# Kernel tuning notes

Hardware: AMD Instinct MI355X
Metric: run time of the kernel (lower is better)

The kernel has to match this reference:

```python
import jax, jax.numpy as jnp
import numpy as np

# ---- statevector quantum-circuit simulation helpers ----

def _rx(theta):
    # RX gate; theta scalar -> [2,2], theta [T] -> [T,2,2]
    c = jnp.cos(theta / 2.0).astype(jnp.complex64)
    s = (-1j * jnp.sin(theta / 2.0)).astype(jnp.complex64)
    return jnp.stack([jnp.stack([c, s], -1), jnp.stack([s, c], -1)], -2)


def _rot(phi, theta, omega):
    # PennyLane Rot = RZ(omega) RY(theta) RZ(phi)
    c = jnp.cos(theta / 2.0).astype(jnp.complex64)
    s = jnp.sin(theta / 2.0).astype(jnp.complex64)
    ep = jnp.exp(-0.5j * (omega + phi)).astype(jnp.complex64)
    em = jnp.exp(0.5j * (omega - phi)).astype(jnp.complex64)
    return jnp.stack([jnp.stack([ep * c, -jnp.conj(em) * s], -1),
                      jnp.stack([em * s, jnp.conj(ep) * c], -1)], -2)


def _apply1(state, gate, wire):
    # state: [T] + [2]*n ; gate: [2,2] (shared) or [T,2,2] (per-token encoding)
    state = jnp.moveaxis(state, 1 + wire, -1)
    if gate.ndim == 3:
        state = jnp.einsum('t...a,tba->t...b', state, gate)
    else:
        state = jnp.einsum('...a,ba->...b', state, gate)
    return jnp.moveaxis(state, -1, 1 + wire)


def _cnot(state, c, t):
    st = jnp.moveaxis(state, (1 + c, 1 + t), (-2, -1))
    st = jnp.stack([st[..., 0, :], st[..., 1, ::-1]], axis=-2)
    return jnp.moveaxis(st, (-2, -1), (1 + c, 1 + t))


def _zexp(state, wire):
    p = state.real ** 2 + state.imag ** 2
    p = jnp.moveaxis(p, 1 + wire, -1).reshape(p.shape[0], -1, 2)
    return jnp.sum(p[..., 0] - p[..., 1], axis=1)


def _qcircuit(x, w, scalar_out):
    # x: [T, n] angle-encoded inputs; w: [3n] (+1 if scalar_out) trainable angles
    T, n = x.shape
    state = jnp.zeros((T,) + (2,) * n, jnp.complex64)
    state = state.at[(slice(None),) + (0,) * n].set(1.0)
    for i in range(n):                       # angle encoding
        state = _apply1(state, _rx(x[:, i]), i)
    if n > 1:                                # ring entanglement
        for i in range(n):
            state = _cnot(state, i, (i + 1) % n)
    for i in range(n):                       # trainable rotations
        state = _apply1(state, _rot(w[3 * i], w[3 * i + 1], w[3 * i + 2]), i)
    if scalar_out:                           # query/key: extra RX, measure Z on wire 0
        state = _apply1(state, _rx(w[3 * n]), 0)
        return _zexp(state, 0)
    return jnp.stack([_zexp(state, i) for i in range(n)], axis=-1)


def _layernorm(x, eps=1e-5):
    m = jnp.mean(x, -1, keepdims=True)
    v = jnp.mean((x - m) ** 2, -1, keepdims=True)
    return (x - m) / jnp.sqrt(v + eps)


def setup_inputs() -> dict:
    key = jax.random.key(0)
    k = jax.random.split(key, 5)
    B, S, E, H = 16, 512, 8, 2
    d = E // H
    return {
        'x': jax.random.normal(k[0], (B, S, E), jnp.float32),
        'Vw': jax.random.normal(k[1], (H, 3 * d), jnp.float32),
        'Qw': jax.random.normal(k[2], (H, 3 * d + 1), jnp.float32),
        'Kw': jax.random.normal(k[3], (H, 3 * d + 1), jnp.float32),
        'Mw': jax.random.normal(k[4], (3 * E,), jnp.float32),
    }


def reference(x, Vw, Qw, Kw, Mw):
    B, S, E = x.shape
    H = Vw.shape[0]
    d = E // H
    scale = 1.0 / np.sqrt(d).astype(np.float32)
    xn = _layernorm(x)
    outs = []
    for h in range(H):  # fixed small loop over structurally distinct heads
        xh = xn[..., h * d:(h + 1) * d].reshape(B * S, d)
        V = _qcircuit(xh, Vw[h], False).reshape(B, S, d)
        Q = _qcircuit(xh, Qw[h], True).reshape(B, S)
        K = _qcircuit(xh, Kw[h], True).reshape(B, S)
        A = -(Q[:, :, None] - K[:, None, :]) ** 2          # [B,S,S]
        P = jax.nn.softmax(A * scale, axis=-1)
        outs.append(jnp.einsum('bij,bjd->bid', P, V))
    head_out = jnp.concatenate(outs, axis=-1)              # [B,S,E]
    merged = _qcircuit(head_out.reshape(B * S, E), Mw, False).reshape(B, S, E)
    return merged + x
```

## Files before the change

### kernel.cpp

```cpp
#include <hip/hip_runtime.h>

#define NS 512


__global__ __launch_bounds__(256)
void k_attn(const float* __restrict__ x, const float* __restrict__ Vw,
            const float* __restrict__ Qw, const float* __restrict__ Kw,
            float* __restrict__ HO)
{
    __shared__ float Qs[NS];
    __shared__ float Ks[NS];
    __shared__ float4 Vs[NS];

    int blk = blockIdx.x;
    int rg = blk & 31;
    int b  = (blk >> 5) & 15;
    int h  = blk >> 9;
    int tid = threadIdx.x;

    const float* qw = Qw + h*13;
    const float* kw = Kw + h*13;
    const float* vw = Vw + h*12;
    float sT, cT, sB, cB;
    __sincosf(qw[1], &sT, &cT); __sincosf(qw[12], &sB, &cB);
    float aQ = cB*cT + sB*sT*__sinf(qw[2]);
    __sincosf(kw[1], &sT, &cT); __sincosf(kw[12], &sB, &cB);
    float aK = cB*cT + sB*sT*__sinf(kw[2]);
    float vc0 = __cosf(vw[1]);
    float vc1 = __cosf(vw[4]);
    float vc2 = __cosf(vw[7]);
    float s3, vc3; __sincosf(vw[10], &s3, &vc3);
    float vs3 = s3 * __sinf(vw[9]);

    #pragma unroll
    for (int k = 0; k < 2; ++k) {
        int tl = tid + k*256;
        const float4* xp = (const float4*)(x + (b*NS + tl)*8);
        float4 xa = xp[0], xb = xp[1];
        float xv[8] = {xa.x, xa.y, xa.z, xa.w, xb.x, xb.y, xb.z, xb.w};
        float m = 0.f;
        #pragma unroll
        for (int e = 0; e < 8; ++e) m += xv[e];
        m *= 0.125f;
        float var = 0.f;
        #pragma unroll
        for (int e = 0; e < 8; ++e) { float d = xv[e]-m; var += d*d; }
        float inv = rsqrtf(var*0.125f + 1e-5f);

        float cg[4], sg[4];
        #pragma unroll
        for (int i = 0; i < 4; ++i)
            __sincosf((xv[h*4+i]-m)*inv, &sg[i], &cg[i]);

        float c01  = cg[0]*cg[1];
        float c123 = cg[1]*cg[2]*cg[3];
        Qs[tl] = aQ * c123;
        Ks[tl] = aK * c123;
        float4 v;
        v.x = vc0 * c123;
        v.y = vc1 * c01;
        v.z = vc2 * c01 * cg[2];
        v.w = vc3 * c01 * cg[2] * cg[3] + vs3 * sg[0]*sg[1]*sg[3]*cg[2];
        Vs[tl] = v;
    }
    __syncthreads();

    int lane = tid & 63;
    int w = tid >> 6;
    int g = lane >> 4;
    int l16 = lane & 15;
    int i = rg*16 + w*4 + g;
    float q = Qs[i];

    float sum = 0.f, a0 = 0.f, a1 = 0.f, a2 = 0.f, a3 = 0.f;
    #pragma unroll
    for (int k = 0; k < 32; ++k) {
        int j = k*16 + l16;
        float d = q - Ks[j];
        float p = __expf(-0.5f*d*d);
        float4 vv = Vs[j];
        sum += p; a0 += p*vv.x; a1 += p*vv.y; a2 += p*vv.z; a3 += p*vv.w;
    }
    #pragma unroll
    for (int off = 1; off < 16; off <<= 1) {
        sum += __shfl_xor(sum, off, 16);
        a0  += __shfl_xor(a0,  off, 16);
        a1  += __shfl_xor(a1,  off, 16);
        a2  += __shfl_xor(a2,  off, 16);
        a3  += __shfl_xor(a3,  off, 16);
    }
    if (l16 == 0) {
        float r = 1.0f / sum;
        float4 o = {a0*r, a1*r, a2*r, a3*r};
        *((float4*)(HO + ((b*NS + i))*8 + h*4)) = o;
    }
}

__global__ __launch_bounds__(64)
void k_merge(const float* __restrict__ HO, const float* __restrict__ x,
             const float* __restrict__ Mw, float* __restrict__ out)
{
    int t = blockIdx.x * 64 + threadIdx.x;

    float cT0 = __cosf(Mw[1]);
    float cT1 = __cosf(Mw[4]);
    float cT2 = __cosf(Mw[7]);
    float cT3 = __cosf(Mw[10]);
    float cT4 = __cosf(Mw[13]);
    float cT5 = __cosf(Mw[16]);
    float cT6 = __cosf(Mw[19]);
    float s7w, cT7; __sincosf(Mw[22], &s7w, &cT7);
    float vs77 = s7w * __sinf(Mw[21]);

    const float4* hp = (const float4*)(HO + t*8);
    float4 h0 = hp[0], h1 = hp[1];
    float a[8] = {h0.x, h0.y, h0.z, h0.w, h1.x, h1.y, h1.z, h1.w};

    float ca[8], sa0, sa1, sa7;
    __sincosf(a[0], &sa0, &ca[0]);
    __sincosf(a[1], &sa1, &ca[1]);
    ca[2] = __cosf(a[2]);
    ca[3] = __cosf(a[3]);
    ca[4] = __cosf(a[4]);
    ca[5] = __cosf(a[5]);
    ca[6] = __cosf(a[6]);
    __sincosf(a[7], &sa7, &ca[7]);

    float P1 = ca[0]*ca[1];
    float P2 = P1*ca[2];
    float P3 = P2*ca[3];
    float P4 = P3*ca[4];
    float P5 = P4*ca[5];
    float P6 = P5*ca[6];
    float P7 = P6*ca[7];
    float c34 = ca[3]*ca[4], c56 = ca[5]*ca[6];
    float Q17 = ca[1]*ca[2]*c34*c56*ca[7];
    float M26 = ca[2]*c34*c56;

    float e0 = cT0*Q17;
    float e1 = cT1*P1;
    float e2 = cT2*P2;
    float e3 = cT3*P3;
    float e4 = cT4*P4;
    float e5 = cT5*P5;
    float e6 = cT6*P6;
    float e7 = cT7*P7 + vs77 * sa0*sa1*sa7*M26;

    const float4* xp = (const float4*)(x + t*8);
    float4 x0 = xp[0], x1 = xp[1];
    float4 o0 = {e0 + x0.x, e1 + x0.y, e2 + x0.z, e3 + x0.w};
    float4 o1 = {e4 + x1.x, e5 + x1.y, e6 + x1.z, e7 + x1.w};
    float4* op = (float4*)(out + t*8);
    op[0] = o0; op[1] = o1;
}

extern "C" void kernel_launch(void* const* d_in, const int* in_sizes, int n_in,
                              void* d_out, int out_size, void* d_ws, size_t ws_size,
                              hipStream_t stream) {
    (void)in_sizes; (void)n_in; (void)out_size; (void)ws_size;
    const float* x  = (const float*)d_in[0];
    const float* Vw = (const float*)d_in[1];
    const float* Qw = (const float*)d_in[2];
    const float* Kw = (const float*)d_in[3];
    const float* Mw = (const float*)d_in[4];
    float* out = (float*)d_out;
    float* HO  = (float*)d_ws;

    hipLaunchKernelGGL(k_attn,  dim3(1024), dim3(256), 0, stream, x, Vw, Qw, Kw, HO);
    hipLaunchKernelGGL(k_merge, dim3(128),  dim3(64),  0, stream, HO, x, Mw, out);
}
```

Measured before the change: 12.70 us.

## Fuse attention heads and merge circuit into a single kernel

Combines the two attention heads and the merge quantum circuit into one kernel. Each block now handles one 16-row group of a batch for both heads, computing Q/K/V for both heads in shared memory and writing head outputs to shared memory instead of a global workspace. The merge circuit and residual add then run in the same block, removing the second launch and the global round trip. In exchange, per-block LDS usage doubles, each row is reduced by 8 lanes instead of 16 with a longer loop, and the merge stage runs on only 16 threads.

```diff
diff --git a/kernel.cpp b/kernel.cpp
--- a/kernel.cpp
+++ b/kernel.cpp
@@ -4,33 +4,36 @@
 
 
 __global__ __launch_bounds__(256)
-void k_attn(const float* __restrict__ x, const float* __restrict__ Vw,
-            const float* __restrict__ Qw, const float* __restrict__ Kw,
-            float* __restrict__ HO)
+void k_fused(const float* __restrict__ x, const float* __restrict__ Vw,
+             const float* __restrict__ Qw, const float* __restrict__ Kw,
+             const float* __restrict__ Mw, float* __restrict__ out)
 {
-    __shared__ float Qs[NS];
-    __shared__ float Ks[NS];
-    __shared__ float4 Vs[NS];
+    __shared__ float  Qs[2][NS];
+    __shared__ float  Ks[2][NS];
+    __shared__ float4 Vs[2][NS];
+    __shared__ float  HOs[16][8];
 
-    int blk = blockIdx.x;
-    int rg = blk & 31;
-    int b  = (blk >> 5) & 15;
-    int h  = blk >> 9;
     int tid = threadIdx.x;
+    int b   = blockIdx.x >> 5;
+    int rg  = blockIdx.x & 31;
 
-    const float* qw = Qw + h*13;
-    const float* kw = Kw + h*13;
-    const float* vw = Vw + h*12;
-    float sT, cT, sB, cB;
-    __sincosf(qw[1], &sT, &cT); __sincosf(qw[12], &sB, &cB);
-    float aQ = cB*cT + sB*sT*__sinf(qw[2]);
-    __sincosf(kw[1], &sT, &cT); __sincosf(kw[12], &sB, &cB);
-    float aK = cB*cT + sB*sT*__sinf(kw[2]);
-    float vc0 = __cosf(vw[1]);
-    float vc1 = __cosf(vw[4]);
-    float vc2 = __cosf(vw[7]);
-    float s3, vc3; __sincosf(vw[10], &s3, &vc3);
-    float vs3 = s3 * __sinf(vw[9]);
+    float aQ[2], aK[2], vc0[2], vc1[2], vc2[2], vc3[2], vs3[2];
+    #pragma unroll
+    for (int h = 0; h < 2; ++h) {
+        const float* qw = Qw + h*13;
+        const float* kw = Kw + h*13;
+        const float* vw = Vw + h*12;
+        float sT, cT, sB, cB;
+        __sincosf(qw[1], &sT, &cT); __sincosf(qw[12], &sB, &cB);
+        aQ[h] = cB*cT + sB*sT*__sinf(qw[2]);
+        __sincosf(kw[1], &sT, &cT); __sincosf(kw[12], &sB, &cB);
+        aK[h] = cB*cT + sB*sT*__sinf(kw[2]);
+        vc0[h] = __cosf(vw[1]);
+        vc1[h] = __cosf(vw[4]);
+        vc2[h] = __cosf(vw[7]);
+        float s3; __sincosf(vw[10], &s3, &vc3[h]);
+        vs3[h] = s3 * __sinf(vw[9]);
+    }
 
     #pragma unroll
     for (int k = 0; k < 2; ++k) {
@@ -47,125 +50,121 @@
         for (int e = 0; e < 8; ++e) { float d = xv[e]-m; var += d*d; }
         float inv = rsqrtf(var*0.125f + 1e-5f);
 
-        float cg[4], sg[4];
         #pragma unroll
-        for (int i = 0; i < 4; ++i)
-            __sincosf((xv[h*4+i]-m)*inv, &sg[i], &cg[i]);
-
-        float c01  = cg[0]*cg[1];
-        float c123 = cg[1]*cg[2]*cg[3];
-        Qs[tl] = aQ * c123;
-        Ks[tl] = aK * c123;
-        float4 v;
-        v.x = vc0 * c123;
-        v.y = vc1 * c01;
-        v.z = vc2 * c01 * cg[2];
-        v.w = vc3 * c01 * cg[2] * cg[3] + vs3 * sg[0]*sg[1]*sg[3]*cg[2];
-        Vs[tl] = v;
+        for (int h = 0; h < 2; ++h) {
+            float cg[4], sg[4];
+            #pragma unroll
+            for (int i = 0; i < 4; ++i)
+                __sincosf((xv[h*4+i]-m)*inv, &sg[i], &cg[i]);
+            float c01  = cg[0]*cg[1];
+            float c123 = cg[1]*cg[2]*cg[3];
+            Qs[h][tl] = aQ[h] * c123;
+            Ks[h][tl] = aK[h] * c123;
+            float4 v;
+            v.x = vc0[h] * c123;
+            v.y = vc1[h] * c01;
+            v.z = vc2[h] * c01 * cg[2];
+            v.w = vc3[h] * c01 * cg[2] * cg[3] + vs3[h] * sg[0]*sg[1]*sg[3]*cg[2];
+            Vs[h][tl] = v;
+        }
     }
     __syncthreads();
 
-    int lane = tid & 63;
-    int w = tid >> 6;
-    int g = lane >> 4;
-    int l16 = lane & 15;
-    int i = rg*16 + w*4 + g;
-    float q = Qs[i];
+    {
+        int lane = tid & 63;
+        int w    = tid >> 6;
+        int task = w*8 + (lane >> 3);
+        int l8   = lane & 7;
+        int hh   = task >> 4;
+        int r    = task & 15;
+        int row  = rg*16 + r;
+        float q  = Qs[hh][row];
 
-    float sum = 0.f, a0 = 0.f, a1 = 0.f, a2 = 0.f, a3 = 0.f;
-    #pragma unroll
-    for (int k = 0; k < 32; ++k) {
-        int j = k*16 + l16;
-        float d = q - Ks[j];
-        float p = __expf(-0.5f*d*d);
-        float4 vv = Vs[j];
-        sum += p; a0 += p*vv.x; a1 += p*vv.y; a2 += p*vv.z; a3 += p*vv.w;
+        float sum = 0.f, a0 = 0.f, a1 = 0.f, a2 = 0.f, a3 = 0.f;
+        #pragma unroll 8
+        for (int k = 0; k < 64; ++k) {
+            int j = k*8 + l8;
+            float d = q - Ks[hh][j];
+            float p = __expf(-0.5f*d*d);
+            float4 vv = Vs[hh][j];
+            sum += p; a0 += p*vv.x; a1 += p*vv.y; a2 += p*vv.z; a3 += p*vv.w;
+        }
+        #pragma unroll
+        for (int off = 1; off < 8; off <<= 1) {
+            sum += __shfl_xor(sum, off, 8);
+            a0  += __shfl_xor(a0,  off, 8);
+            a1  += __shfl_xor(a1,  off, 8);
+            a2  += __shfl_xor(a2,  off, 8);
+            a3  += __shfl_xor(a3,  off, 8);
+        }
+        if (l8 == 0) {
+            float rr = 1.0f / sum;
+            HOs[r][hh*4 + 0] = a0*rr;
+            HOs[r][hh*4 + 1] = a1*rr;
+            HOs[r][hh*4 + 2] = a2*rr;
+            HOs[r][hh*4 + 3] = a3*rr;
+        }
     }
-    #pragma unroll
-    for (int off = 1; off < 16; off <<= 1) {
-        sum += __shfl_xor(sum, off, 16);
-        a0  += __shfl_xor(a0,  off, 16);
-        a1  += __shfl_xor(a1,  off, 16);
-        a2  += __shfl_xor(a2,  off, 16);
-        a3  += __shfl_xor(a3,  off, 16);
+    __syncthreads();
+
+    if (tid < 16) {
+        float cT0 = __cosf(Mw[1]);
+        float cT1 = __cosf(Mw[4]);
+        float cT2 = __cosf(Mw[7]);
+        float cT3 = __cosf(Mw[10]);
+        float cT4 = __cosf(Mw[13]);
+        float cT5 = __cosf(Mw[16]);
+        float cT6 = __cosf(Mw[19]);
+        float s7w, cT7; __sincosf(Mw[22], &s7w, &cT7);
+        float vs77 = s7w * __sinf(Mw[21]);
+
+        int t = b*NS + rg*16 + tid;
+        float a[8];
+        #pragma unroll
+        for (int e = 0; e < 8; ++e) a[e] = HOs[tid][e];
+
+        float ca[8], sa0, sa1, sa7;
+        __sincosf(a[0], &sa0, &ca[0]);
+        __sincosf(a[1], &sa1, &ca[1]);
+        ca[2] = __cosf(a[2]);
+        ca[3] = __cosf(a[3]);
+        ca[4] = __cosf(a[4]);
+        ca[5] = __cosf(a[5]);
+        ca[6] = __cosf(a[6]);
+        __sincosf(a[7], &sa7, &ca[7]);
+
+        float P1 = ca[0]*ca[1];
+        float P2 = P1*ca[2];
+        float P3 = P2*ca[3];
+        float P4 = P3*ca[4];
+        float P5 = P4*ca[5];
+        float P6 = P5*ca[6];
+        float P7 = P6*ca[7];
+        float c34 = ca[3]*ca[4], c56 = ca[5]*ca[6];
+        float Q17 = ca[1]*ca[2]*c34*c56*ca[7];
+        float M26 = ca[2]*c34*c56;
+
+        const float4* xp = (const float4*)(x + t*8);
+        float4 x0 = xp[0], x1 = xp[1];
+        float4 o0 = {cT0*Q17 + x0.x, cT1*P1 + x0.y, cT2*P2 + x0.z, cT3*P3 + x0.w};
+        float4 o1 = {cT4*P4 + x1.x, cT5*P5 + x1.y, cT6*P6 + x1.z,
+                     cT7*P7 + vs77*sa0*sa1*sa7*M26 + x1.w};
+        float4* op = (float4*)(out + t*8);
+        op[0] = o0; op[1] = o1;
     }
-    if (l16 == 0) {
-        float r = 1.0f / sum;
-        float4 o = {a0*r, a1*r, a2*r, a3*r};
-        *((float4*)(HO + ((b*NS + i))*8 + h*4)) = o;
-    }
-}
-
-__global__ __launch_bounds__(64)
-void k_merge(const float* __restrict__ HO, const float* __restrict__ x,
-             const float* __restrict__ Mw, float* __restrict__ out)
-{
-    int t = blockIdx.x * 64 + threadIdx.x;
-
-    float cT0 = __cosf(Mw[1]);
-    float cT1 = __cosf(Mw[4]);
-    float cT2 = __cosf(Mw[7]);
-    float cT3 = __cosf(Mw[10]);
-    float cT4 = __cosf(Mw[13]);
-    float cT5 = __cosf(Mw[16]);
-    float cT6 = __cosf(Mw[19]);
-    float s7w, cT7; __sincosf(Mw[22], &s7w, &cT7);
-    float vs77 = s7w * __sinf(Mw[21]);
-
-    const float4* hp = (const float4*)(HO + t*8);
-    float4 h0 = hp[0], h1 = hp[1];
-    float a[8] = {h0.x, h0.y, h0.z, h0.w, h1.x, h1.y, h1.z, h1.w};
-
-    float ca[8], sa0, sa1, sa7;
-    __sincosf(a[0], &sa0, &ca[0]);
-    __sincosf(a[1], &sa1, &ca[1]);
-    ca[2] = __cosf(a[2]);
-    ca[3] = __cosf(a[3]);
-    ca[4] = __cosf(a[4]);
-    ca[5] = __cosf(a[5]);
-    ca[6] = __cosf(a[6]);
-    __sincosf(a[7], &sa7, &ca[7]);
-
-    float P1 = ca[0]*ca[1];
-    float P2 = P1*ca[2];
-    float P3 = P2*ca[3];
-    float P4 = P3*ca[4];
-    float P5 = P4*ca[5];
-    float P6 = P5*ca[6];
-    float P7 = P6*ca[7];
-    float c34 = ca[3]*ca[4], c56 = ca[5]*ca[6];
-    float Q17 = ca[1]*ca[2]*c34*c56*ca[7];
-    float M26 = ca[2]*c34*c56;
-
-    float e0 = cT0*Q17;
-    float e1 = cT1*P1;
-    float e2 = cT2*P2;
-    float e3 = cT3*P3;
-    float e4 = cT4*P4;
-    float e5 = cT5*P5;
-    float e6 = cT6*P6;
-    float e7 = cT7*P7 + vs77 * sa0*sa1*sa7*M26;
-
-    const float4* xp = (const float4*)(x + t*8);
-    float4 x0 = xp[0], x1 = xp[1];
-    float4 o0 = {e0 + x0.x, e1 + x0.y, e2 + x0.z, e3 + x0.w};
-    float4 o1 = {e4 + x1.x, e5 + x1.y, e6 + x1.z, e7 + x1.w};
-    float4* op = (float4*)(out + t*8);
-    op[0] = o0; op[1] = o1;
 }
 
 extern "C" void kernel_launch(void* const* d_in, const int* in_sizes, int n_in,
                               void* d_out, int out_size, void* d_ws, size_t ws_size,
                               hipStream_t stream) {
-    (void)in_sizes; (void)n_in; (void)out_size; (void)ws_size;
+    (void)in_sizes; (void)n_in; (void)out_size; (void)d_ws; (void)ws_size;
     const float* x  = (const float*)d_in[0];
     const float* Vw = (const float*)d_in[1];
     const float* Qw = (const float*)d_in[2];
     const float* Kw = (const float*)d_in[3];
     const float* Mw = (const float*)d_in[4];
     float* out = (float*)d_out;
-    float* HO  = (float*)d_ws;
 
-    hipLaunchKernelGGL(k_attn,  dim3(1024), dim3(256), 0, stream, x, Vw, Qw, Kw, HO);
-    hipLaunchKernelGGL(k_merge, dim3(128),  dim3(64),  0, stream, HO, x, Mw, out);
+    hipLaunchKernelGGL(k_fused, dim3(512), dim3(256), 0, stream,
+                       x, Vw, Qw, Kw, Mw, out);
 }
```

Result: faster. 11.35 us (-10.7%).
